# Kernel optimization log

Measured on AMD Instinct MI355X. Metric: run time of the kernel, lower is better.

The kernel has to match this reference:

```python
import jax, jax.numpy as jnp
import numpy as np

K = 3  # kernel size (hardcoded in module defaults; padding=1, stride=1, dilation=1)


def conv2d(x, w, b, pad=1):
    # x: [B,C,H,W], w: [O,C,kh,kw]
    out = jax.lax.conv_general_dilated(
        x, w, window_strides=(1, 1), padding=[(pad, pad), (pad, pad)],
        dimension_numbers=("NCHW", "OIHW", "NCHW"))
    return out + b[None, :, None, None]


def _bilinear_sample(img, py, px):
    # img: [C,H,W]; py, px: [K*K,Ho,Wo] float sample coords.
    # Zero-padded bilinear sampling (matches torchvision deform_conv2d):
    # each of the 4 corner taps contributes 0 if it lies outside the image.
    H, W = img.shape[1], img.shape[2]
    y0 = jnp.floor(py)
    x0 = jnp.floor(px)
    y1, x1 = y0 + 1.0, x0 + 1.0
    wy1 = py - y0
    wy0 = 1.0 - wy1
    wx1 = px - x0
    wx0 = 1.0 - wx1

    def corner(y, x):
        yi = jnp.clip(y.astype(jnp.int32), 0, H - 1)
        xi = jnp.clip(x.astype(jnp.int32), 0, W - 1)
        valid = ((y >= 0) & (y <= H - 1) & (x >= 0) & (x <= W - 1))
        return img[:, yi, xi] * valid.astype(img.dtype)[None]  # [C,K*K,Ho,Wo]

    return (corner(y0, x0) * (wy0 * wx0)[None]
            + corner(y0, x1) * (wy0 * wx1)[None]
            + corner(y1, x0) * (wy1 * wx0)[None]
            + corner(y1, x1) * (wy1 * wx1)[None])


def setup_inputs() -> dict:
    key = jax.random.key(0)
    ks = jax.random.split(key, 4)
    B, C, O, H, W = 8, 128, 256, 96, 96
    x = jax.random.normal(ks[0], (B, C, H, W), dtype=jnp.float32)
    # scale offset/mask conv weights so learned offsets stay a few pixels
    offset_w = jax.random.normal(ks[1], (2 * K * K, C, K, K), dtype=jnp.float32) * 0.01
    offset_b = jnp.zeros((2 * K * K,), dtype=jnp.float32)
    mask_w = jax.random.normal(ks[2], (K * K, C, K, K), dtype=jnp.float32) * 0.05
    mask_b = jnp.zeros((K * K,), dtype=jnp.float32)
    weight = jax.random.normal(ks[3], (O, C, K, K), dtype=jnp.float32) * 0.05
    bias = jnp.zeros((O,), dtype=jnp.float32)
    return {"x": x, "offset_w": offset_w, "offset_b": offset_b,
            "mask_w": mask_w, "mask_b": mask_b, "weight": weight, "bias": bias}


def reference(x, offset_w, offset_b, mask_w, mask_b, weight, bias):
    B, C, H, W = x.shape
    O = weight.shape[0]
    pad = 1
    offset = conv2d(x, offset_w, offset_b, pad)              # [B,2*K*K,H,W]
    mask = jax.nn.sigmoid(conv2d(x, mask_w, mask_b, pad))    # [B,K*K,H,W]
    Ho, Wo = offset.shape[2], offset.shape[3]

    # base sampling grid: output pixel - pad + kernel tap position
    kh, kw = jnp.meshgrid(jnp.arange(K), jnp.arange(K), indexing="ij")
    kh = kh.reshape(-1).astype(x.dtype)  # [K*K]
    kw = kw.reshape(-1).astype(x.dtype)
    base_y = (jnp.arange(Ho, dtype=x.dtype)[None, :, None] - pad
              + kh[:, None, None])                           # [K*K,Ho,1]
    base_x = (jnp.arange(Wo, dtype=x.dtype)[None, None, :] - pad
              + kw[:, None, None])                           # [K*K,1,Wo]

    # torchvision layout: channel 2k = y-offset, 2k+1 = x-offset for tap k
    off = offset.reshape(B, K * K, 2, Ho, Wo)
    py = base_y[None] + off[:, :, 0]                         # [B,K*K,Ho,Wo]
    px = base_x[None] + off[:, :, 1]

    samples = jax.vmap(_bilinear_sample)(x, py, px)          # [B,C,K*K,Ho,Wo]
    w_flat = weight.reshape(O, C, K * K)
    out = jnp.einsum("bckhw,bkhw,ock->bohw", samples, mask, w_flat)
    return out + bias[None, :, None, None]
```

## Files before the change

kernel.cpp:

```cpp
#include <hip/hip_runtime.h>

#define CIN 128
#define COUT 256
#define IH 96
#define IW 96
#define NB 8
#define HW (IH*IW)
#define NPIX (NB*HW)
#define AST 136
#define BLK_PER_IMG (HW/64)
#define TBLK (NPIX/64)

typedef __attribute__((ext_vector_type(8))) short short8;
typedef __attribute__((ext_vector_type(4))) float floatx4;

static __device__ __forceinline__ short f2bf(float f) {
  unsigned int u = __builtin_bit_cast(unsigned int, f);
  u = u + 0x7fffu + ((u >> 16) & 1u);
  return (short)(u >> 16);
}
static __device__ __forceinline__ float bf2f(short s) {
  unsigned int u = ((unsigned int)(unsigned short)s) << 16;
  return __builtin_bit_cast(float, u);
}

struct Corner {
  float w00, w01, w10, w11;
  const short *r00, *r01, *r10, *r11;
};

static __device__ __forceinline__ Corner corner_setup(float py, float px, float mk,
                                                      const short* xtb, int choff) {
  Corner c;
  float y0f = floorf(py), x0f = floorf(px);
  float wy1 = py - y0f, wx1 = px - x0f;
  float wy0 = 1.f - wy1, wx0 = 1.f - wx1;
  bool vy0 = (y0f >= 0.f) && (y0f <= (float)(IH - 1));
  bool vy1 = (y0f + 1.f >= 0.f) && (y0f + 1.f <= (float)(IH - 1));
  bool vx0 = (x0f >= 0.f) && (x0f <= (float)(IW - 1));
  bool vx1 = (x0f + 1.f >= 0.f) && (x0f + 1.f <= (float)(IW - 1));
  int iy0 = min(max((int)y0f, 0), IH - 1);
  int iy1 = min(max((int)y0f + 1, 0), IH - 1);
  int ix0 = min(max((int)x0f, 0), IW - 1);
  int ix1 = min(max((int)x0f + 1, 0), IW - 1);
  c.w00 = wy0 * wx0 * mk * ((vy0 && vx0) ? 1.f : 0.f);
  c.w01 = wy0 * wx1 * mk * ((vy0 && vx1) ? 1.f : 0.f);
  c.w10 = wy1 * wx0 * mk * ((vy1 && vx0) ? 1.f : 0.f);
  c.w11 = wy1 * wx1 * mk * ((vy1 && vx1) ? 1.f : 0.f);
  c.r00 = xtb + (size_t)(iy0 * IW + ix0) * 128 + choff;
  c.r01 = xtb + (size_t)(iy0 * IW + ix1) * 128 + choff;
  c.r10 = xtb + (size_t)(iy1 * IW + ix0) * 128 + choff;
  c.r11 = xtb + (size_t)(iy1 * IW + ix1) * 128 + choff;
  return c;
}

static __device__ __forceinline__ short8 interp8(short8 s00, short8 s01,
                                                 short8 s10, short8 s11,
                                                 const Corner& c) {
  short8 o;
  #pragma unroll
  for (int j = 0; j < 8; ++j) {
    float v = c.w00 * bf2f(s00[j]) + c.w01 * bf2f(s01[j])
            + c.w10 * bf2f(s10[j]) + c.w11 * bf2f(s11[j]);
    o[j] = f2bf(v);
  }
  return o;
}

__global__ __launch_bounds__(256, 8)
void prep_and_transpose(const float* __restrict__ x, short* __restrict__ xt,
                        const float* __restrict__ weight,
                        const float* __restrict__ offset_w,
                        const float* __restrict__ mask_w,
                        short* __restrict__ Bt2f, short* __restrict__ Bt1f) {
  const int blk = blockIdx.x;
  const int tid = threadIdx.x;

  if (blk >= TBLK) {
    const int n2 = 9 * 4 * 16 * 512;
    int base = (blk - TBLK) * 1024 + tid;
    #pragma unroll
    for (int k = 0; k < 4; ++k) {
      int idx = base + k * 256;
      if (idx < n2) {
        int e = idx & 7, lane = (idx >> 3) & 63;
        int g = idx >> 9;
        int nl = g & 15, kq = (g >> 4) & 3, tap = g >> 6;
        int o = nl * 16 + (lane & 15);
        int c = kq * 32 + (lane >> 4) * 8 + e;
        Bt2f[idx] = f2bf(weight[(o * CIN + c) * 9 + tap]);
      } else {
        int j = idx - n2;
        int e = j & 7, lane = (j >> 3) & 63;
        int g = j >> 9;
        int nl = g & 1, kq = (g >> 1) & 3, tap = g >> 3;
        int n = nl * 16 + (lane & 15);
        int c = kq * 32 + (lane >> 4) * 8 + e;
        float v = 0.f;
        if (n < 27)
          v = (n < 18) ? offset_w[(n * CIN + c) * 9 + tap]
                       : mask_w[((n - 18) * CIN + c) * 9 + tap];
        Bt1f[j] = f2bf(v);
      }
    }
    return;
  }

  __shared__ short tile[64 * 130];
  const int p0  = blk * 64;
  const int b   = p0 / HW;
  const int hw0 = p0 % HW;
  const float* xb = x + (size_t)b * CIN * HW + hw0;

  const int pq = tid & 15;
  const int cg = tid >> 4;

  #pragma unroll
  for (int r = 0; r < 4; ++r) {
    const int c = r * 32 + cg * 2;
    float4 v0 = *(const float4*)(xb + (size_t)c * HW + 4 * pq);
    float4 v1 = *(const float4*)(xb + (size_t)(c + 1) * HW + 4 * pq);
    unsigned int d0 = (unsigned short)f2bf(v0.x) | ((unsigned int)(unsigned short)f2bf(v1.x) << 16);
    unsigned int d1 = (unsigned short)f2bf(v0.y) | ((unsigned int)(unsigned short)f2bf(v1.y) << 16);
    unsigned int d2 = (unsigned short)f2bf(v0.z) | ((unsigned int)(unsigned short)f2bf(v1.z) << 16);
    unsigned int d3 = (unsigned short)f2bf(v0.w) | ((unsigned int)(unsigned short)f2bf(v1.w) << 16);
    *(unsigned int*)(&tile[(4 * pq + 0) * 130 + c]) = d0;
    *(unsigned int*)(&tile[(4 * pq + 1) * 130 + c]) = d1;
    *(unsigned int*)(&tile[(4 * pq + 2) * 130 + c]) = d2;
    *(unsigned int*)(&tile[(4 * pq + 3) * 130 + c]) = d3;
  }
  __syncthreads();

  unsigned int* dst = (unsigned int*)(xt + ((size_t)b * HW + hw0) * 128);
  #pragma unroll
  for (int i = 0; i < 4; ++i) {
    int gidx = i * 1024 + tid * 4;
    int px = gidx >> 6, cw0 = gidx & 63;
    uint4 w;
    w.x = *(const unsigned int*)(&tile[px * 130 + 2 * (cw0 + 0)]);
    w.y = *(const unsigned int*)(&tile[px * 130 + 2 * (cw0 + 1)]);
    w.z = *(const unsigned int*)(&tile[px * 130 + 2 * (cw0 + 2)]);
    w.w = *(const unsigned int*)(&tile[px * 130 + 2 * (cw0 + 3)]);
    *(uint4*)(dst + gidx) = w;
  }
}

__global__ __launch_bounds__(256, 3)
void deform_main(const short* __restrict__ xt,
                 const short* __restrict__ Bt2f,
                 const short* __restrict__ Bt1f,
                 const float* __restrict__ offset_b,
                 const float* __restrict__ mask_b,
                 const float* __restrict__ bias,
                 float* __restrict__ out) {
  __shared__ short Ald[2][64 * AST];
  __shared__ float pmb[27 * 65];

  const int tid  = threadIdx.x;
  const int lane = tid & 63;
  const int wv   = tid >> 6;
  const int q    = lane >> 4;
  const int m    = lane & 15;
  const int blk  = blockIdx.x;
  const int l    = (blk & 7) * BLK_PER_IMG + (blk >> 3);
  const int p0   = l * 64;
  const int b    = p0 / HW;
  const short* xtb = xt + (size_t)b * HW * 128;

  {
    const int p  = p0 + wv * 16 + m;
    const int hw = p % HW;
    const int h  = hw / IW, w_ = hw % IW;

    floatx4 acc0 = (floatx4){0.f, 0.f, 0.f, 0.f};
    floatx4 acc1 = (floatx4){0.f, 0.f, 0.f, 0.f};

    for (int tap = 0; tap < 9; ++tap) {
      const int kh = tap / 3, kw = tap % 3;
      const int iy = h + kh - 1, ix = w_ + kw - 1;
      const bool vald = (iy >= 0 && iy < IH && ix >= 0 && ix < IW);
      const size_t pbase = vald ? (size_t)(iy * IW + ix) * 128 : 0;

      short8 a[4], bb0[4], bb1[4];
      #pragma unroll
      for (int kq = 0; kq < 4; ++kq)
        a[kq] = *(const short8*)(xtb + pbase + kq * 32 + q * 8);
      #pragma unroll
      for (int kq = 0; kq < 4; ++kq) {
        bb0[kq] = *(const short8*)(Bt1f + (size_t)((tap * 4 + kq) * 2 + 0) * 512 + lane * 8);
        bb1[kq] = *(const short8*)(Bt1f + (size_t)((tap * 4 + kq) * 2 + 1) * 512 + lane * 8);
      }
      #pragma unroll
      for (int kq = 0; kq < 4; ++kq) {
        short8 av = a[kq];
        if (!vald) av = (short8){0, 0, 0, 0, 0, 0, 0, 0};
        acc0 = __builtin_amdgcn_mfma_f32_16x16x32_bf16(av, bb0[kq], acc0, 0, 0, 0);
        acc1 = __builtin_amdgcn_mfma_f32_16x16x32_bf16(av, bb1[kq], acc1, 0, 0, 0);
      }
    }

    #pragma unroll
    for (int nl = 0; nl < 2; ++nl) {
      floatx4 ac = nl ? acc1 : acc0;
      int ch = nl * 16 + m;
      if (ch < 18) {
        int tap = ch >> 1, plane = ch & 1;
        float cb = offset_b[ch];
        #pragma unroll
        for (int r = 0; r < 4; ++r) {
          int col = wv * 16 + q * 4 + r;
          int hwp = (p0 + col) % HW;
          float base = plane ? (float)(hwp % IW + tap % 3 - 1)
                             : (float)(hwp / IW + tap / 3 - 1);
          pmb[(plane * 9 + tap) * 65 + col] = ac[r] + cb + base;
        }
      } else if (ch < 27) {
        int tap = ch - 18;
        float cb = mask_b[tap];
        #pragma unroll
        for (int r = 0; r < 4; ++r) {
          int col = wv * 16 + q * 4 + r;
          float v = ac[r] + cb;
          pmb[(18 + tap) * 65 + col] = 1.f / (1.f + expf(-v));
        }
      }
    }
  }
  __syncthreads();

  const int r8    = lane >> 3;
  const int ck    = lane & 7;
  const int ckoff = ck * 8;
  const int row0  = wv * 16 + r8;
  const int row1  = row0 + 8;
  const int wk0   = (row0 >> 1) & 7;
  const int wk1   = (row1 >> 1) & 7;
  const int wb0   = row0 * AST;
  const int wb1   = row1 * AST;
  const int rsw   = (m >> 1) & 7;

  floatx4 acc[4][4];
  #pragma unroll
  for (int i = 0; i < 4; ++i)
    #pragma unroll
    for (int j = 0; j < 4; ++j) acc[i][j] = (floatx4){0.f, 0.f, 0.f, 0.f};

  {
    float py0 = pmb[row0], px0 = pmb[9 * 65 + row0], mk0 = pmb[18 * 65 + row0];
    float py1 = pmb[row1], px1 = pmb[9 * 65 + row1], mk1 = pmb[18 * 65 + row1];
    Corner c0 = corner_setup(py0, px0, mk0, xtb, ckoff);
    Corner c1 = corner_setup(py1, px1, mk1, xtb, ckoff);
    short8 a0 = *(const short8*)(c0.r00),      a1 = *(const short8*)(c0.r01);
    short8 a2 = *(const short8*)(c0.r10),      a3 = *(const short8*)(c0.r11);
    short8 a4 = *(const short8*)(c0.r00 + 64), a5 = *(const short8*)(c0.r01 + 64);
    short8 a6 = *(const short8*)(c0.r10 + 64), a7 = *(const short8*)(c0.r11 + 64);
    short8 b0 = *(const short8*)(c1.r00),      b1 = *(const short8*)(c1.r01);
    short8 b2 = *(const short8*)(c1.r10),      b3 = *(const short8*)(c1.r11);
    short8 b4 = *(const short8*)(c1.r00 + 64), b5 = *(const short8*)(c1.r01 + 64);
    short8 b6 = *(const short8*)(c1.r10 + 64), b7 = *(const short8*)(c1.r11 + 64);
    *(short8*)(&Ald[0][wb0 + (ck ^ wk0) * 8])       = interp8(a0, a1, a2, a3, c0);
    *(short8*)(&Ald[0][wb0 + (8 + (ck ^ wk0)) * 8]) = interp8(a4, a5, a6, a7, c0);
    *(short8*)(&Ald[0][wb1 + (ck ^ wk1) * 8])       = interp8(b0, b1, b2, b3, c1);
    *(short8*)(&Ald[0][wb1 + (8 + (ck ^ wk1)) * 8]) = interp8(b4, b5, b6, b7, c1);
  }
  float pyN0 = pmb[1 * 65 + row0];
  float pxN0 = pmb[10 * 65 + row0];
  float mkN0 = pmb[19 * 65 + row0];
  float pyN1 = pmb[1 * 65 + row1];
  float pxN1 = pmb[10 * 65 + row1];
  float mkN1 = pmb[19 * 65 + row1];
  __syncthreads();

  for (int tap = 0; tap < 9; ++tap) {
    const short* bufr = Ald[tap & 1];
    short* const wbuf = Ald[(tap & 1) ^ 1];
    const bool nxt = (tap < 8);

    Corner c0, c1;
    if (nxt) {
      c0 = corner_setup(pyN0, pxN0, mkN0, xtb, ckoff);
      c1 = corner_setup(pyN1, pxN1, mkN1, xtb, ckoff);
    }
    if (tap < 7) {
      pyN0 = pmb[(tap + 2) * 65 + row0];
      pxN0 = pmb[(tap + 11) * 65 + row0];
      mkN0 = pmb[(tap + 20) * 65 + row0];
      pyN1 = pmb[(tap + 2) * 65 + row1];
      pxN1 = pmb[(tap + 11) * 65 + row1];
      mkN1 = pmb[(tap + 20) * 65 + row1];
    }

    short8 bfA[4], bfB[4];
    #pragma unroll
    for (int nl = 0; nl < 4; ++nl) {
      bfA[nl] = *(const short8*)(Bt2f + (size_t)((tap * 4 + 0) * 16 + wv * 4 + nl) * 512 + lane * 8);
      bfB[nl] = *(const short8*)(Bt2f + (size_t)((tap * 4 + 1) * 16 + wv * 4 + nl) * 512 + lane * 8);
    }
    short8 g0, g1, g2, g3, g4, g5, g6, g7;
    if (nxt) {
      g0 = *(const short8*)(c0.r00);      g1 = *(const short8*)(c0.r01);
      g2 = *(const short8*)(c0.r10);      g3 = *(const short8*)(c0.r11);
      g4 = *(const short8*)(c0.r00 + 64); g5 = *(const short8*)(c0.r01 + 64);
      g6 = *(const short8*)(c0.r10 + 64); g7 = *(const short8*)(c0.r11 + 64);
    }
    {
      short8 af[4];
      #pragma unroll
      for (int mt = 0; mt < 4; ++mt)
        af[mt] = *(const short8*)(bufr + (mt * 16 + m) * AST + ((0 * 4 + q) ^ rsw) * 8);
      #pragma unroll
      for (int mt = 0; mt < 4; ++mt)
        #pragma unroll
        for (int nl = 0; nl < 4; ++nl)
          acc[mt][nl] = __builtin_amdgcn_mfma_f32_16x16x32_bf16(af[mt], bfA[nl], acc[mt][nl], 0, 0, 0);
    }
    {
      short8 af[4];
      #pragma unroll
      for (int mt = 0; mt < 4; ++mt)
        af[mt] = *(const short8*)(bufr + (mt * 16 + m) * AST + ((1 * 4 + q) ^ rsw) * 8);
      #pragma unroll
      for (int mt = 0; mt < 4; ++mt)
        #pragma unroll
        for (int nl = 0; nl < 4; ++nl)
          acc[mt][nl] = __builtin_amdgcn_mfma_f32_16x16x32_bf16(af[mt], bfB[nl], acc[mt][nl], 0, 0, 0);
    }
    short8 bfC[4], bfD[4];
    #pragma unroll
    for (int nl = 0; nl < 4; ++nl) {
      bfC[nl] = *(const short8*)(Bt2f + (size_t)((tap * 4 + 2) * 16 + wv * 4 + nl) * 512 + lane * 8);
      bfD[nl] = *(const short8*)(Bt2f + (size_t)((tap * 4 + 3) * 16 + wv * 4 + nl) * 512 + lane * 8);
    }
    if (nxt) {
      *(short8*)(&wbuf[wb0 + (ck ^ wk0) * 8])       = interp8(g0, g1, g2, g3, c0);
      *(short8*)(&wbuf[wb0 + (8 + (ck ^ wk0)) * 8]) = interp8(g4, g5, g6, g7, c0);
      g0 = *(const short8*)(c1.r00);      g1 = *(const short8*)(c1.r01);
      g2 = *(const short8*)(c1.r10);      g3 = *(const short8*)(c1.r11);
      g4 = *(const short8*)(c1.r00 + 64); g5 = *(const short8*)(c1.r01 + 64);
      g6 = *(const short8*)(c1.r10 + 64); g7 = *(const short8*)(c1.r11 + 64);
    }
    {
      short8 af[4];
      #pragma unroll
      for (int mt = 0; mt < 4; ++mt)
        af[mt] = *(const short8*)(bufr + (mt * 16 + m) * AST + ((2 * 4 + q) ^ rsw) * 8);
      #pragma unroll
      for (int mt = 0; mt < 4; ++mt)
        #pragma unroll
        for (int nl = 0; nl < 4; ++nl)
          acc[mt][nl] = __builtin_amdgcn_mfma_f32_16x16x32_bf16(af[mt], bfC[nl], acc[mt][nl], 0, 0, 0);
    }
    {
      short8 af[4];
      #pragma unroll
      for (int mt = 0; mt < 4; ++mt)
        af[mt] = *(const short8*)(bufr + (mt * 16 + m) * AST + ((3 * 4 + q) ^ rsw) * 8);
      #pragma unroll
      for (int mt = 0; mt < 4; ++mt)
        #pragma unroll
        for (int nl = 0; nl < 4; ++nl)
          acc[mt][nl] = __builtin_amdgcn_mfma_f32_16x16x32_bf16(af[mt], bfD[nl], acc[mt][nl], 0, 0, 0);
    }
    if (nxt) {
      *(short8*)(&wbuf[wb1 + (ck ^ wk1) * 8])       = interp8(g0, g1, g2, g3, c1);
      *(short8*)(&wbuf[wb1 + (8 + (ck ^ wk1)) * 8]) = interp8(g4, g5, g6, g7, c1);
      __syncthreads();
    }
  }

  const int hw0 = p0 % HW;
  #pragma unroll
  for (int nl = 0; nl < 4; ++nl) {
    const int o = wv * 64 + nl * 16 + m;
    const float bs = bias[o];
    float* op = out + (size_t)(b * COUT + o) * HW + hw0;
    #pragma unroll
    for (int mt = 0; mt < 4; ++mt) {
      floatx4 v = acc[mt][nl];
      v[0] += bs; v[1] += bs; v[2] += bs; v[3] += bs;
      *(floatx4*)(op + mt * 16 + q * 4) = v;
    }
  }
}

extern "C" void kernel_launch(void* const* d_in, const int* in_sizes, int n_in,
                              void* d_out, int out_size, void* d_ws, size_t ws_size,
                              hipStream_t stream) {
  const float* x        = (const float*)d_in[0];
  const float* offset_w = (const float*)d_in[1];
  const float* offset_b = (const float*)d_in[2];
  const float* mask_w   = (const float*)d_in[3];
  const float* mask_b   = (const float*)d_in[4];
  const float* weight   = (const float*)d_in[5];
  const float* bias     = (const float*)d_in[6];
  float* out = (float*)d_out;

  char* ws = (char*)d_ws;
  const size_t XT_BYTES  = (size_t)NPIX * 128 * 2;
  const size_t BT2_BYTES = (size_t)9 * 4 * 16 * 512 * 2;
  short* xtp  = (short*)ws;
  short* Bt2f = (short*)(ws + XT_BYTES);
  short* Bt1f = (short*)(ws + XT_BYTES + BT2_BYTES);

  prep_and_transpose<<<dim3(TBLK + 324), dim3(256), 0, stream>>>(
      x, xtp, weight, offset_w, mask_w, Bt2f, Bt1f);
  deform_main<<<dim3(NPIX / 64), dim3(256), 0, stream>>>(
      xtp, Bt2f, Bt1f, offset_b, mask_b, bias, out);
}
```

Baseline: 217.6 us.

## Stage offset-conv taps through LDS with chunk-major layout and raise occupancy

```diff
diff --git a/kernel.cpp b/kernel.cpp
--- a/kernel.cpp
+++ b/kernel.cpp
@@ -7,9 +7,10 @@
 #define NB 8
 #define HW (IH*IW)
 #define NPIX (NB*HW)
-#define AST 136
 #define BLK_PER_IMG (HW/64)
 #define TBLK (NPIX/64)
+#define ALD_CS 528
+#define ALD_BUF (16*ALD_CS)
 
 typedef __attribute__((ext_vector_type(8))) short short8;
 typedef __attribute__((ext_vector_type(4))) float floatx4;
@@ -145,7 +146,7 @@
   }
 }
 
-__global__ __launch_bounds__(256, 3)
+__global__ __launch_bounds__(256, 4)
 void deform_main(const short* __restrict__ xt,
                  const short* __restrict__ Bt2f,
                  const short* __restrict__ Bt1f,
@@ -153,91 +154,115 @@
                  const float* __restrict__ mask_b,
                  const float* __restrict__ bias,
                  float* __restrict__ out) {
-  __shared__ short Ald[2][64 * AST];
-  __shared__ float pmb[27 * 65];
+  __shared__ short Ald[2 * ALD_BUF];
+  __shared__ float pmb[64 * 27];
 
   const int tid  = threadIdx.x;
   const int lane = tid & 63;
   const int wv   = tid >> 6;
   const int q    = lane >> 4;
   const int m    = lane & 15;
+  const int r8   = lane >> 3;
+  const int ck   = lane & 7;
+  const int ckoff = ck * 8;
   const int blk  = blockIdx.x;
   const int l    = (blk & 7) * BLK_PER_IMG + (blk >> 3);
   const int p0   = l * 64;
   const int b    = p0 / HW;
   const short* xtb = xt + (size_t)b * HW * 128;
 
+  const int row0 = wv * 16 + r8;
+  const int row1 = row0 + 8;
+
+  const int hw0p = (p0 + row0) % HW;
+  const int h0p  = hw0p / IW, w0p = hw0p % IW;
+  const int hw1p = (p0 + row1) % HW;
+  const int h1p  = hw1p / IW, w1p = hw1p % IW;
+
   {
-    const int p  = p0 + wv * 16 + m;
-    const int hw = p % HW;
-    const int h  = hw / IW, w_ = hw % IW;
-
+    const short8 z = (short8){0, 0, 0, 0, 0, 0, 0, 0};
     floatx4 acc0 = (floatx4){0.f, 0.f, 0.f, 0.f};
     floatx4 acc1 = (floatx4){0.f, 0.f, 0.f, 0.f};
+    short8 P0, P1, P2, P3;
+
+    auto ldtap = [&](int tap, short8& A0, short8& A1, short8& B0, short8& B1) {
+      const int kh = tap / 3, kw = tap % 3;
+      int iy = h0p + kh - 1, ix = w0p + kw - 1;
+      bool v = (iy >= 0) && (iy < IH) && (ix >= 0) && (ix < IW);
+      const short* s = xtb + (v ? (size_t)(iy * IW + ix) * 128 : 0) + ckoff;
+      A0 = *(const short8*)(s);
+      A1 = *(const short8*)(s + 64);
+      if (!v) { A0 = z; A1 = z; }
+      iy = h1p + kh - 1; ix = w1p + kw - 1;
+      bool v2 = (iy >= 0) && (iy < IH) && (ix >= 0) && (ix < IW);
+      const short* s2 = xtb + (v2 ? (size_t)(iy * IW + ix) * 128 : 0) + ckoff;
+      B0 = *(const short8*)(s2);
+      B1 = *(const short8*)(s2 + 64);
+      if (!v2) { B0 = z; B1 = z; }
+    };
+    auto sttap = [&](short* buf, short8 A0, short8 A1, short8 B0, short8 B1) {
+      *(short8*)(&buf[ck * ALD_CS + row0 * 8])       = A0;
+      *(short8*)(&buf[(ck + 8) * ALD_CS + row0 * 8]) = A1;
+      *(short8*)(&buf[ck * ALD_CS + row1 * 8])       = B0;
+      *(short8*)(&buf[(ck + 8) * ALD_CS + row1 * 8]) = B1;
+    };
+
+    ldtap(0, P0, P1, P2, P3);
+    sttap(Ald, P0, P1, P2, P3);
+    __syncthreads();
 
     for (int tap = 0; tap < 9; ++tap) {
-      const int kh = tap / 3, kw = tap % 3;
-      const int iy = h + kh - 1, ix = w_ + kw - 1;
-      const bool vald = (iy >= 0 && iy < IH && ix >= 0 && ix < IW);
-      const size_t pbase = vald ? (size_t)(iy * IW + ix) * 128 : 0;
-
-      short8 a[4], bb0[4], bb1[4];
-      #pragma unroll
-      for (int kq = 0; kq < 4; ++kq)
-        a[kq] = *(const short8*)(xtb + pbase + kq * 32 + q * 8);
+      const short* rb = Ald + (tap & 1) * ALD_BUF;
+      short* const wb2 = Ald + ((tap & 1) ^ 1) * ALD_BUF;
+      if (tap < 8) ldtap(tap + 1, P0, P1, P2, P3);
+
+      short8 bb0[4], bb1[4];
       #pragma unroll
       for (int kq = 0; kq < 4; ++kq) {
         bb0[kq] = *(const short8*)(Bt1f + (size_t)((tap * 4 + kq) * 2 + 0) * 512 + lane * 8);
         bb1[kq] = *(const short8*)(Bt1f + (size_t)((tap * 4 + kq) * 2 + 1) * 512 + lane * 8);
       }
+      short8 a[4];
+      #pragma unroll
+      for (int kq = 0; kq < 4; ++kq)
+        a[kq] = *(const short8*)(&rb[(kq * 4 + q) * ALD_CS + (wv * 16 + m) * 8]);
       #pragma unroll
       for (int kq = 0; kq < 4; ++kq) {
-        short8 av = a[kq];
-        if (!vald) av = (short8){0, 0, 0, 0, 0, 0, 0, 0};
-        acc0 = __builtin_amdgcn_mfma_f32_16x16x32_bf16(av, bb0[kq], acc0, 0, 0, 0);
-        acc1 = __builtin_amdgcn_mfma_f32_16x16x32_bf16(av, bb1[kq], acc1, 0, 0, 0);
+        acc0 = __builtin_amdgcn_mfma_f32_16x16x32_bf16(a[kq], bb0[kq], acc0, 0, 0, 0);
+        acc1 = __builtin_amdgcn_mfma_f32_16x16x32_bf16(a[kq], bb1[kq], acc1, 0, 0, 0);
       }
+      if (tap < 8) sttap(wb2, P0, P1, P2, P3);
+      __syncthreads();
     }
 
     #pragma unroll
     for (int nl = 0; nl < 2; ++nl) {
       floatx4 ac = nl ? acc1 : acc0;
-      int ch = nl * 16 + m;
-      if (ch < 18) {
-        int tap = ch >> 1, plane = ch & 1;
-        float cb = offset_b[ch];
+      int chn = nl * 16 + m;
+      if (chn < 18) {
+        int tap = chn >> 1, plane = chn & 1;
+        float cb = offset_b[chn];
         #pragma unroll
         for (int r = 0; r < 4; ++r) {
           int col = wv * 16 + q * 4 + r;
           int hwp = (p0 + col) % HW;
           float base = plane ? (float)(hwp % IW + tap % 3 - 1)
                              : (float)(hwp / IW + tap / 3 - 1);
-          pmb[(plane * 9 + tap) * 65 + col] = ac[r] + cb + base;
+          pmb[col * 27 + plane * 9 + tap] = ac[r] + cb + base;
         }
-      } else if (ch < 27) {
-        int tap = ch - 18;
+      } else if (chn < 27) {
+        int tap = chn - 18;
         float cb = mask_b[tap];
         #pragma unroll
         for (int r = 0; r < 4; ++r) {
           int col = wv * 16 + q * 4 + r;
           float v = ac[r] + cb;
-          pmb[(18 + tap) * 65 + col] = 1.f / (1.f + expf(-v));
+          pmb[col * 27 + 18 + tap] = 1.f / (1.f + expf(-v));
         }
       }
     }
   }
   __syncthreads();
-
-  const int r8    = lane >> 3;
-  const int ck    = lane & 7;
-  const int ckoff = ck * 8;
-  const int row0  = wv * 16 + r8;
-  const int row1  = row0 + 8;
-  const int wk0   = (row0 >> 1) & 7;
-  const int wk1   = (row1 >> 1) & 7;
-  const int wb0   = row0 * AST;
-  const int wb1   = row1 * AST;
-  const int rsw   = (m >> 1) & 7;
 
   floatx4 acc[4][4];
   #pragma unroll
@@ -246,8 +271,8 @@
     for (int j = 0; j < 4; ++j) acc[i][j] = (floatx4){0.f, 0.f, 0.f, 0.f};
 
   {
-    float py0 = pmb[row0], px0 = pmb[9 * 65 + row0], mk0 = pmb[18 * 65 + row0];
-    float py1 = pmb[row1], px1 = pmb[9 * 65 + row1], mk1 = pmb[18 * 65 + row1];
+    float py0 = pmb[row0 * 27 + 0], px0 = pmb[row0 * 27 + 9], mk0 = pmb[row0 * 27 + 18];
+    float py1 = pmb[row1 * 27 + 0], px1 = pmb[row1 * 27 + 9], mk1 = pmb[row1 * 27 + 18];
     Corner c0 = corner_setup(py0, px0, mk0, xtb, ckoff);
     Corner c1 = corner_setup(py1, px1, mk1, xtb, ckoff);
     short8 a0 = *(const short8*)(c0.r00),      a1 = *(const short8*)(c0.r01);
@@ -258,22 +283,18 @@
     short8 b2 = *(const short8*)(c1.r10),      b3 = *(const short8*)(c1.r11);
     short8 b4 = *(const short8*)(c1.r00 + 64), b5 = *(const short8*)(c1.r01 + 64);
     short8 b6 = *(const short8*)(c1.r10 + 64), b7 = *(const short8*)(c1.r11 + 64);
-    *(short8*)(&Ald[0][wb0 + (ck ^ wk0) * 8])       = interp8(a0, a1, a2, a3, c0);
-    *(short8*)(&Ald[0][wb0 + (8 + (ck ^ wk0)) * 8]) = interp8(a4, a5, a6, a7, c0);
-    *(short8*)(&Ald[0][wb1 + (ck ^ wk1) * 8])       = interp8(b0, b1, b2, b3, c1);
-    *(short8*)(&Ald[0][wb1 + (8 + (ck ^ wk1)) * 8]) = interp8(b4, b5, b6, b7, c1);
-  }
-  float pyN0 = pmb[1 * 65 + row0];
-  float pxN0 = pmb[10 * 65 + row0];
-  float mkN0 = pmb[19 * 65 + row0];
-  float pyN1 = pmb[1 * 65 + row1];
-  float pxN1 = pmb[10 * 65 + row1];
-  float mkN1 = pmb[19 * 65 + row1];
+    *(short8*)(&Ald[ck * ALD_CS + row0 * 8])       = interp8(a0, a1, a2, a3, c0);
+    *(short8*)(&Ald[(ck + 8) * ALD_CS + row0 * 8]) = interp8(a4, a5, a6, a7, c0);
+    *(short8*)(&Ald[ck * ALD_CS + row1 * 8])       = interp8(b0, b1, b2, b3, c1);
+    *(short8*)(&Ald[(ck + 8) * ALD_CS + row1 * 8]) = interp8(b4, b5, b6, b7, c1);
+  }
+  float pyN0 = pmb[row0 * 27 + 1], pxN0 = pmb[row0 * 27 + 10], mkN0 = pmb[row0 * 27 + 19];
+  float pyN1 = pmb[row1 * 27 + 1], pxN1 = pmb[row1 * 27 + 10], mkN1 = pmb[row1 * 27 + 19];
   __syncthreads();
 
   for (int tap = 0; tap < 9; ++tap) {
-    const short* bufr = Ald[tap & 1];
-    short* const wbuf = Ald[(tap & 1) ^ 1];
+    const short* bufr = Ald + (tap & 1) * ALD_BUF;
+    short* const bufw = Ald + ((tap & 1) ^ 1) * ALD_BUF;
     const bool nxt = (tap < 8);
 
     Corner c0, c1;
@@ -282,12 +303,12 @@
       c1 = corner_setup(pyN1, pxN1, mkN1, xtb, ckoff);
     }
     if (tap < 7) {
-      pyN0 = pmb[(tap + 2) * 65 + row0];
-      pxN0 = pmb[(tap + 11) * 65 + row0];
-      mkN0 = pmb[(tap + 20) * 65 + row0];
-      pyN1 = pmb[(tap + 2) * 65 + row1];
-      pxN1 = pmb[(tap + 11) * 65 + row1];
-      mkN1 = pmb[(tap + 20) * 65 + row1];
+      pyN0 = pmb[row0 * 27 + tap + 2];
+      pxN0 = pmb[row0 * 27 + tap + 11];
+      mkN0 = pmb[row0 * 27 + tap + 20];
+      pyN1 = pmb[row1 * 27 + tap + 2];
+      pxN1 = pmb[row1 * 27 + tap + 11];
+      mkN1 = pmb[row1 * 27 + tap + 20];
     }
 
     short8 bfA[4], bfB[4];
@@ -307,7 +328,7 @@
       short8 af[4];
       #pragma unroll
       for (int mt = 0; mt < 4; ++mt)
-        af[mt] = *(const short8*)(bufr + (mt * 16 + m) * AST + ((0 * 4 + q) ^ rsw) * 8);
+        af[mt] = *(const short8*)(&bufr[(0 * 4 + q) * ALD_CS + (mt * 16 + m) * 8]);
       #pragma unroll
       for (int mt = 0; mt < 4; ++mt)
         #pragma unroll
@@ -318,7 +339,7 @@
       short8 af[4];
       #pragma unroll
       for (int mt = 0; mt < 4; ++mt)
-        af[mt] = *(const short8*)(bufr + (mt * 16 + m) * AST + ((1 * 4 + q) ^ rsw) * 8);
+        af[mt] = *(const short8*)(&bufr[(1 * 4 + q) * ALD_CS + (mt * 16 + m) * 8]);
       #pragma unroll
       for (int mt = 0; mt < 4; ++mt)
         #pragma unroll
@@ -332,8 +353,8 @@
       bfD[nl] = *(const short8*)(Bt2f + (size_t)((tap * 4 + 3) * 16 + wv * 4 + nl) * 512 + lane * 8);
     }
     if (nxt) {
-      *(short8*)(&wbuf[wb0 + (ck ^ wk0) * 8])       = interp8(g0, g1, g2, g3, c0);
-      *(short8*)(&wbuf[wb0 + (8 + (ck ^ wk0)) * 8]) = interp8(g4, g5, g6, g7, c0);
+      *(short8*)(&bufw[ck * ALD_CS + row0 * 8])       = interp8(g0, g1, g2, g3, c0);
+      *(short8*)(&bufw[(ck + 8) * ALD_CS + row0 * 8]) = interp8(g4, g5, g6, g7, c0);
       g0 = *(const short8*)(c1.r00);      g1 = *(const short8*)(c1.r01);
       g2 = *(const short8*)(c1.r10);      g3 = *(const short8*)(c1.r11);
       g4 = *(const short8*)(c1.r00 + 64); g5 = *(const short8*)(c1.r01 + 64);
@@ -343,7 +364,7 @@
       short8 af[4];
       #pragma unroll
       for (int mt = 0; mt < 4; ++mt)
-        af[mt] = *(const short8*)(bufr + (mt * 16 + m) * AST + ((2 * 4 + q) ^ rsw) * 8);
+        af[mt] = *(const short8*)(&bufr[(2 * 4 + q) * ALD_CS + (mt * 16 + m) * 8]);
       #pragma unroll
       for (int mt = 0; mt < 4; ++mt)
         #pragma unroll
@@ -354,7 +375,7 @@
       short8 af[4];
       #pragma unroll
       for (int mt = 0; mt < 4; ++mt)
-        af[mt] = *(const short8*)(bufr + (mt * 16 + m) * AST + ((3 * 4 + q) ^ rsw) * 8);
+        af[mt] = *(const short8*)(&bufr[(3 * 4 + q) * ALD_CS + (mt * 16 + m) * 8]);
       #pragma unroll
       for (int mt = 0; mt < 4; ++mt)
         #pragma unroll
@@ -362,8 +383,8 @@
           acc[mt][nl] = __builtin_amdgcn_mfma_f32_16x16x32_bf16(af[mt], bfD[nl], acc[mt][nl], 0, 0, 0);
     }
     if (nxt) {
-      *(short8*)(&wbuf[wb1 + (ck ^ wk1) * 8])       = interp8(g0, g1, g2, g3, c1);
-      *(short8*)(&wbuf[wb1 + (8 + (ck ^ wk1)) * 8]) = interp8(g4, g5, g6, g7, c1);
+      *(short8*)(&bufw[ck * ALD_CS + row1 * 8])       = interp8(g0, g1, g2, g3, c1);
+      *(short8*)(&bufw[(ck + 8) * ALD_CS + row1 * 8]) = interp8(g4, g5, g6, g7, c1);
       __syncthreads();
     }
   }
```

Result: slower. 251.5 us (+15.6%).
